# Kernel optimization log

Hardware: AMD Instinct MI355X
Metric: run time of the kernel (lower is better)

Reference implementation:

```python
import jax, jax.numpy as jnp
import numpy as np

B, N, D_IN, D, E, MAXD = 16, 512, 256, 64, 32, 50
LN_EPS = 1e-5

def setup_inputs() -> dict:
    key = jax.random.key(0)
    ks = jax.random.split(key, 24)
    s = lambda fan: 1.0 / np.sqrt(fan)
    inp = {
        'x': jax.random.normal(ks[0], (B, N, D_IN), jnp.float32),
        'price_rising_ranks': jax.random.randint(ks[1], (B, N), 0, N, jnp.int64),
        'Wp': jax.random.normal(ks[2], (D_IN, D), jnp.float32) * s(D_IN),
        'bp': jnp.zeros((D,), jnp.float32),
        'Wq': jax.random.normal(ks[3], (D, D), jnp.float32) * s(D),
        'bq': jnp.zeros((D,), jnp.float32),
        'Wk': jax.random.normal(ks[4], (D, D), jnp.float32) * s(D),
        'bk': jnp.zeros((D,), jnp.float32),
        'Wv': jax.random.normal(ks[5], (D, D), jnp.float32) * s(D),
        'bv': jnp.zeros((D,), jnp.float32),
        'Eemb': jax.random.normal(ks[6], (MAXD + 1, E), jnp.float32),
        'Wr1': jax.random.normal(ks[7], (E, 16), jnp.float32) * s(E),
        'br1': jnp.zeros((16,), jnp.float32),
        'Wr2': jax.random.normal(ks[8], (16, 1), jnp.float32) * s(16),
        'Wf1': jax.random.normal(ks[9], (D, 2 * D), jnp.float32) * s(D),
        'bf1': jnp.zeros((2 * D,), jnp.float32),
        'Wf2': jax.random.normal(ks[10], (2 * D, D), jnp.float32) * s(2 * D),
        'bf2': jnp.zeros((D,), jnp.float32),
        'ln_g': jnp.ones((D,), jnp.float32),
        'ln_b': jnp.zeros((D,), jnp.float32),
        'Ws1': jax.random.normal(ks[11], (D, 32), jnp.float32) * s(D),
        'bs1': jnp.zeros((32,), jnp.float32),
        'Ws2': jax.random.normal(ks[12], (32, 1), jnp.float32) * s(32),
        'bs2': jnp.zeros((1,), jnp.float32),
    }
    return inp

def reference(x, price_rising_ranks, Wp, bp, Wq, bq, Wk, bk, Wv, bv,
              Eemb, Wr1, br1, Wr2, Wf1, bf1, Wf2, bf2, ln_g, ln_b,
              Ws1, bs1, Ws2, bs2):
    xp = x @ Wp + bp                                  # (B,N,D)
    q = xp @ Wq + bq
    k = xp @ Wk + bk
    v = xp @ Wv + bv
    scores = jnp.einsum('bnd,bmd->bnm', q, k) / jnp.sqrt(jnp.float32(D))
    # rank-distance pairwise bias
    r = price_rising_ranks
    dists = jnp.clip(jnp.abs(r[:, :, None] - r[:, None, :]), 0, MAXD)  # (B,N,N) int
    emb = Eemb[dists]                                 # (B,N,N,E)
    w = jax.nn.relu(emb @ Wr1 + br1) @ Wr2            # (B,N,N,1)
    rel = jax.nn.sigmoid(w[..., 0])                   # (B,N,N)
    scores = scores * rel
    attn = jax.nn.softmax(scores, axis=-1)
    ao = jnp.einsum('bnm,bmd->bnd', attn, v)
    # feed forward + layernorm
    h = jax.nn.relu(ao @ Wf1 + bf1) @ Wf2 + bf2
    mu = jnp.mean(h, axis=-1, keepdims=True)
    var = jnp.mean((h - mu) ** 2, axis=-1, keepdims=True)
    hn = (h - mu) / jnp.sqrt(var + LN_EPS) * ln_g + ln_b
    # score projection
    out = jax.nn.relu(hn @ Ws1 + bs1) @ Ws2 + bs2     # (B,N,1)
    return jax.nn.sigmoid(out[..., 0])                # (B,N)
```

## Files before the change

### kernel.cpp

```cpp
#include <hip/hip_runtime.h>

using f32x4 = __attribute__((ext_vector_type(4))) float;
using s16x8 = __attribute__((ext_vector_type(8))) short;

static __device__ __forceinline__ unsigned short f2bf(float f){
  union { float f; unsigned int i; } c; c.f = f;
  return (unsigned short)((c.i + 0x7FFFu + ((c.i >> 16) & 1u)) >> 16);
}
static __device__ __forceinline__ s16x8 ld8(const unsigned short* p){
  return *(const s16x8*)p;
}
static __device__ __forceinline__ s16x8 cvt8(const float* p){
  const float4* q = (const float4*)p;
  float4 a = q[0], b = q[1];
  s16x8 r;
  r[0]=(short)f2bf(a.x); r[1]=(short)f2bf(a.y); r[2]=(short)f2bf(a.z); r[3]=(short)f2bf(a.w);
  r[4]=(short)f2bf(b.x); r[5]=(short)f2bf(b.y); r[6]=(short)f2bf(b.z); r[7]=(short)f2bf(b.w);
  return r;
}
static __device__ __forceinline__ f32x4 mfma16(s16x8 a, s16x8 b, f32x4 c){
  return __builtin_amdgcn_mfma_f32_16x16x32_bf16(a, b, c, 0, 0, 0);
}

__global__ __launch_bounds__(64) void k_prep(const float* __restrict__ Ee,
    const float* __restrict__ Wr1, const float* __restrict__ br1,
    const float* __restrict__ Wr2, float* __restrict__ rel_t)
{
  int t = threadIdx.x;
  if (t < 51){
    float e[32];
    for (int j = 0; j < 32; ++j) e[j] = Ee[t*32 + j];
    float w = 0.f;
    for (int h = 0; h < 16; ++h){
      float s = br1[h];
      for (int j = 0; j < 32; ++j) s += e[j] * Wr1[j*16 + h];
      s = fmaxf(s, 0.f);
      w += s * Wr2[h];
    }
    rel_t[t] = 1.f / (1.f + __expf(-w));
  }
}

__global__ __launch_bounds__(256) void k_xp(const float* __restrict__ x,
    const float* __restrict__ Wp, const float* __restrict__ bp,
    unsigned short* __restrict__ xp)
{
  __shared__ __align__(16) unsigned short Wt[64*264];
  int t = threadIdx.x;
  for (int i = t; i < 256*64; i += 256){
    int k = i >> 6, n = i & 63;
    Wt[n*264 + k] = f2bf(Wp[i]);
  }
  __syncthreads();
  int lane = t & 63, wave = t >> 6;
  int colL = lane & 15, quad = lane >> 4;
  int row0 = blockIdx.x * 64 + wave * 16;
  const float* xr = x + (row0 + colL)*256;
  f32x4 acc[4] = {};
  for (int kc = 0; kc < 256; kc += 32){
    s16x8 a = cvt8(xr + kc + quad*8);
#pragma unroll
    for (int nt = 0; nt < 4; ++nt){
      s16x8 b = ld8(&Wt[(nt*16 + colL)*264 + kc + quad*8]);
      acc[nt] = mfma16(a, b, acc[nt]);
    }
  }
#pragma unroll
  for (int nt = 0; nt < 4; ++nt){
    int col = nt*16 + colL;
    float bias = bp[col];
#pragma unroll
    for (int i = 0; i < 4; ++i){
      int row = row0 + quad*4 + i;
      xp[row*64 + col] = f2bf(acc[nt][i] + bias);
    }
  }
}

__global__ __launch_bounds__(256) void k_qkv(const unsigned short* __restrict__ xp,
    const float* __restrict__ Wq, const float* __restrict__ bq,
    const float* __restrict__ Wk, const float* __restrict__ bk,
    const float* __restrict__ Wv, const float* __restrict__ bv,
    unsigned short* __restrict__ q, unsigned short* __restrict__ k, unsigned short* __restrict__ vt)
{
  int which = blockIdx.y;
  const float* W    = which==0 ? Wq : (which==1 ? Wk : Wv);
  const float* bias = which==0 ? bq : (which==1 ? bk : bv);
  __shared__ __align__(16) unsigned short Wt[64*72];
  int t = threadIdx.x;
  for (int i = t; i < 64*64; i += 256){
    int kx = i >> 6, n = i & 63;
    Wt[n*72 + kx] = f2bf(W[i]);
  }
  __syncthreads();
  int lane = t & 63, wave = t >> 6;
  int colL = lane & 15, quad = lane >> 4;
  int row0 = blockIdx.x*64 + wave*16;
  f32x4 acc[4] = {};
#pragma unroll
  for (int kc = 0; kc < 64; kc += 32){
    s16x8 a = ld8(xp + (row0+colL)*64 + kc + quad*8);
#pragma unroll
    for (int nt = 0; nt < 4; ++nt){
      s16x8 b = ld8(&Wt[(nt*16+colL)*72 + kc + quad*8]);
      acc[nt] = mfma16(a, b, acc[nt]);
    }
  }
#pragma unroll
  for (int nt = 0; nt < 4; ++nt){
    int col = nt*16 + colL;
    float bb = bias[col];
#pragma unroll
    for (int i = 0; i < 4; ++i){
      int row = row0 + quad*4 + i;
      float v = acc[nt][i] + bb;
      if (which == 0)      q[row*64 + col] = f2bf(v);
      else if (which == 1) k[row*64 + col] = f2bf(v);
      else                 vt[(row>>9)*32768 + col*512 + (row & 511)] = f2bf(v);
    }
  }
}

__global__ __launch_bounds__(128) void k_attn(const unsigned short* __restrict__ q,
    const unsigned short* __restrict__ kmat, const unsigned short* __restrict__ vt,
    const int* __restrict__ ranks, const float* __restrict__ rel_t,
    unsigned short* __restrict__ ao)
{
  int b = blockIdx.y, qb = blockIdx.x;
  int t = threadIdx.x;
  int lane = t & 63, wave = t >> 6;
  int colL = lane & 15, quad = lane >> 4;

  __shared__ int r_s[512];
  __shared__ float rt_s[64];
  __shared__ __align__(16) unsigned short P[2][16*520];

  for (int i = t; i < 512; i += 128) r_s[i] = ranks[b*512 + i];
  if (t < 64) rt_s[t] = (t < 51) ? rel_t[t] : 0.f;
  __syncthreads();

  int row0 = qb*32 + wave*16;
  const unsigned short* qp = q    + b*512*64;
  const unsigned short* kp = kmat + b*512*64;
  const unsigned short* vp = vt   + b*64*512;

  s16x8 aq0 = ld8(qp + (row0+colL)*64 +  0 + quad*8);
  s16x8 aq1 = ld8(qp + (row0+colL)*64 + 32 + quad*8);

  f32x4 S[32];
#pragma unroll
  for (int mt = 0; mt < 32; ++mt){
    s16x8 b0 = ld8(kp + (mt*16+colL)*64 +  0 + quad*8);
    s16x8 b1 = ld8(kp + (mt*16+colL)*64 + 32 + quad*8);
    f32x4 c = {};
    c = mfma16(aq0, b0, c);
    c = mfma16(aq1, b1, c);
    S[mt] = c;
  }

  int rq[4];
#pragma unroll
  for (int i = 0; i < 4; ++i) rq[i] = r_s[row0 + quad*4 + i];

  float rmax[4] = {-1e30f,-1e30f,-1e30f,-1e30f};
#pragma unroll
  for (int mt = 0; mt < 32; ++mt){
    int rm = r_s[mt*16 + colL];
#pragma unroll
    for (int i = 0; i < 4; ++i){
      int dd = rq[i] - rm; dd = dd < 0 ? -dd : dd; dd = dd > 50 ? 50 : dd;
      float s = S[mt][i] * 0.125f * rt_s[dd];
      S[mt][i] = s;
      rmax[i] = fmaxf(rmax[i], s);
    }
  }
#pragma unroll
  for (int i = 0; i < 4; ++i){
    rmax[i] = fmaxf(rmax[i], __shfl_xor(rmax[i], 1));
    rmax[i] = fmaxf(rmax[i], __shfl_xor(rmax[i], 2));
    rmax[i] = fmaxf(rmax[i], __shfl_xor(rmax[i], 4));
    rmax[i] = fmaxf(rmax[i], __shfl_xor(rmax[i], 8));
  }
  float rsum[4] = {0.f,0.f,0.f,0.f};
#pragma unroll
  for (int mt = 0; mt < 32; ++mt){
#pragma unroll
    for (int i = 0; i < 4; ++i){
      float p = __expf(S[mt][i] - rmax[i]);
      S[mt][i] = p;
      rsum[i] += p;
    }
  }
#pragma unroll
  for (int i = 0; i < 4; ++i){
    rsum[i] += __shfl_xor(rsum[i], 1);
    rsum[i] += __shfl_xor(rsum[i], 2);
    rsum[i] += __shfl_xor(rsum[i], 4);
    rsum[i] += __shfl_xor(rsum[i], 8);
  }
  float inv[4];
#pragma unroll
  for (int i = 0; i < 4; ++i) inv[i] = 1.f / rsum[i];

  unsigned short* Pw = P[wave];
#pragma unroll
  for (int mt = 0; mt < 32; ++mt){
#pragma unroll
    for (int i = 0; i < 4; ++i)
      Pw[(quad*4+i)*520 + mt*16 + colL] = f2bf(S[mt][i] * inv[i]);
  }
  __syncthreads();

  f32x4 O[4] = {};
#pragma unroll
  for (int mc = 0; mc < 512; mc += 32){
    s16x8 ap = ld8(&Pw[colL*520 + mc + quad*8]);
#pragma unroll
    for (int dt = 0; dt < 4; ++dt){
      s16x8 bb = ld8(vp + (dt*16+colL)*512 + mc + quad*8);
      O[dt] = mfma16(ap, bb, O[dt]);
    }
  }
#pragma unroll
  for (int dt = 0; dt < 4; ++dt){
#pragma unroll
    for (int i = 0; i < 4; ++i)
      ao[(b*512 + row0 + quad*4 + i)*64 + dt*16 + colL] = f2bf(O[dt][i]);
  }
}

__global__ __launch_bounds__(256) void k_ffn(const unsigned short* __restrict__ ao,
    const float* __restrict__ Wf1, const float* __restrict__ bf1,
    const float* __restrict__ Wf2, const float* __restrict__ bf2,
    const float* __restrict__ lng, const float* __restrict__ lnb,
    const float* __restrict__ Ws1, const float* __restrict__ bs1,
    const float* __restrict__ Ws2, const float* __restrict__ bs2,
    float* __restrict__ out)
{
  __shared__ __align__(16) unsigned short Wf1t[128*72];
  __shared__ __align__(16) unsigned short Wf2t[64*136];
  __shared__ __align__(16) unsigned short Ws1t[32*72];
  __shared__ __align__(16) unsigned short hbuf[4][16*136];
  __shared__ float cb[384];

  int t = threadIdx.x;
  for (int i = t; i < 64*128; i += 256){ int d = i>>7, j = i&127; Wf1t[j*72 + d] = f2bf(Wf1[i]); }
  for (int i = t; i < 128*64; i += 256){ int kx = i>>6, n = i&63; Wf2t[n*136 + kx] = f2bf(Wf2[i]); }
  for (int i = t; i < 64*32;  i += 256){ int d = i>>5, c = i&31; Ws1t[c*72 + d] = f2bf(Ws1[i]); }
  if (t < 128) cb[t] = bf1[t];
  if (t < 64){ cb[128+t] = bf2[t]; cb[192+t] = lng[t]; cb[256+t] = lnb[t]; }
  if (t < 32){ cb[320+t] = bs1[t]; cb[352+t] = Ws2[t]; }
  __syncthreads();

  int lane = t & 63, wave = t >> 6, colL = lane & 15, quad = lane >> 4;
  int row0 = blockIdx.x*64 + wave*16;
  unsigned short* hw = hbuf[wave];

  f32x4 a1[8] = {};
#pragma unroll
  for (int kc = 0; kc < 64; kc += 32){
    s16x8 a = ld8(ao + (row0+colL)*64 + kc + quad*8);
#pragma unroll
    for (int nt = 0; nt < 8; ++nt){
      s16x8 b = ld8(&Wf1t[(nt*16+colL)*72 + kc + quad*8]);
      a1[nt] = mfma16(a, b, a1[nt]);
    }
  }
#pragma unroll
  for (int nt = 0; nt < 8; ++nt){
    int col = nt*16 + colL;
    float bb = cb[col];
#pragma unroll
    for (int i = 0; i < 4; ++i)
      hw[(quad*4+i)*136 + col] = f2bf(fmaxf(a1[nt][i] + bb, 0.f));
  }
  __syncthreads();

  f32x4 a2[4] = {};
#pragma unroll
  for (int kc = 0; kc < 128; kc += 32){
    s16x8 a = ld8(&hw[colL*136 + kc + quad*8]);
#pragma unroll
    for (int nt = 0; nt < 4; ++nt){
      s16x8 b = ld8(&Wf2t[(nt*16+colL)*136 + kc + quad*8]);
      a2[nt] = mfma16(a, b, a2[nt]);
    }
  }
  float vals[4][4];
#pragma unroll
  for (int nt = 0; nt < 4; ++nt){
    float bb = cb[128 + nt*16 + colL];
#pragma unroll
    for (int i = 0; i < 4; ++i) vals[i][nt] = a2[nt][i] + bb;
  }
  __syncthreads();

  float hnv[4][4];
#pragma unroll
  for (int i = 0; i < 4; ++i){
    float s = vals[i][0]+vals[i][1]+vals[i][2]+vals[i][3];
    s += __shfl_xor(s,1); s += __shfl_xor(s,2); s += __shfl_xor(s,4); s += __shfl_xor(s,8);
    float mu = s * (1.f/64.f);
    float d0=vals[i][0]-mu, d1=vals[i][1]-mu, d2=vals[i][2]-mu, d3=vals[i][3]-mu;
    float s2 = d0*d0 + d1*d1 + d2*d2 + d3*d3;
    s2 += __shfl_xor(s2,1); s2 += __shfl_xor(s2,2); s2 += __shfl_xor(s2,4); s2 += __shfl_xor(s2,8);
    float invs = rsqrtf(s2*(1.f/64.f) + 1e-5f);
#pragma unroll
    for (int nt = 0; nt < 4; ++nt){
      int col = nt*16 + colL;
      hnv[i][nt] = (vals[i][nt]-mu)*invs*cb[192+col] + cb[256+col];
    }
  }
#pragma unroll
  for (int i = 0; i < 4; ++i)
#pragma unroll
    for (int nt = 0; nt < 4; ++nt)
      hw[(quad*4+i)*72 + nt*16 + colL] = f2bf(hnv[i][nt]);
  __syncthreads();

  f32x4 a3[2] = {};
#pragma unroll
  for (int kc = 0; kc < 64; kc += 32){
    s16x8 a = ld8(&hw[colL*72 + kc + quad*8]);
#pragma unroll
    for (int nt = 0; nt < 2; ++nt){
      s16x8 b = ld8(&Ws1t[(nt*16+colL)*72 + kc + quad*8]);
      a3[nt] = mfma16(a, b, a3[nt]);
    }
  }
  float bs2f = bs2[0];
#pragma unroll
  for (int i = 0; i < 4; ++i){
    float p = 0.f;
#pragma unroll
    for (int nt = 0; nt < 2; ++nt){
      int col = nt*16 + colL;
      p += fmaxf(a3[nt][i] + cb[320+col], 0.f) * cb[352+col];
    }
    p += __shfl_xor(p,1); p += __shfl_xor(p,2); p += __shfl_xor(p,4); p += __shfl_xor(p,8);
    if (colL == 0){
      float z = p + bs2f;
      out[row0 + quad*4 + i] = 1.f / (1.f + __expf(-z));
    }
  }
}

extern "C" void kernel_launch(void* const* d_in, const int* in_sizes, int n_in,
                              void* d_out, int out_size, void* d_ws, size_t ws_size,
                              hipStream_t stream)
{
  const float* x    = (const float*)d_in[0];
  const int*   rank = (const int*)d_in[1];
  const float* Wp   = (const float*)d_in[2];
  const float* bp   = (const float*)d_in[3];
  const float* Wq   = (const float*)d_in[4];
  const float* bq   = (const float*)d_in[5];
  const float* Wk   = (const float*)d_in[6];
  const float* bk   = (const float*)d_in[7];
  const float* Wv   = (const float*)d_in[8];
  const float* bv   = (const float*)d_in[9];
  const float* Ee   = (const float*)d_in[10];
  const float* Wr1  = (const float*)d_in[11];
  const float* br1  = (const float*)d_in[12];
  const float* Wr2  = (const float*)d_in[13];
  const float* Wf1  = (const float*)d_in[14];
  const float* bf1  = (const float*)d_in[15];
  const float* Wf2  = (const float*)d_in[16];
  const float* bf2  = (const float*)d_in[17];
  const float* lng  = (const float*)d_in[18];
  const float* lnb  = (const float*)d_in[19];
  const float* Ws1  = (const float*)d_in[20];
  const float* bs1  = (const float*)d_in[21];
  const float* Ws2  = (const float*)d_in[22];
  const float* bs2  = (const float*)d_in[23];
  float* out = (float*)d_out;

  char* ws = (char*)d_ws;
  float*          rel_t = (float*)(ws + 0);
  unsigned short* xp    = (unsigned short*)(ws + 256);
  unsigned short* q     = (unsigned short*)(ws + 256 + 1*1048576);
  unsigned short* kk    = (unsigned short*)(ws + 256 + 2*1048576);
  unsigned short* vt    = (unsigned short*)(ws + 256 + 3*1048576);
  unsigned short* ao    = (unsigned short*)(ws + 256 + 4*1048576);

  k_prep<<<dim3(1), dim3(64), 0, stream>>>(Ee, Wr1, br1, Wr2, rel_t);
  k_xp<<<dim3(128), dim3(256), 0, stream>>>(x, Wp, bp, xp);
  k_qkv<<<dim3(128, 3), dim3(256), 0, stream>>>(xp, Wq, bq, Wk, bk, Wv, bv, q, kk, vt);
  k_attn<<<dim3(16, 16), dim3(128), 0, stream>>>(q, kk, vt, rank, rel_t, ao);
  k_ffn<<<dim3(128), dim3(256), 0, stream>>>(ao, Wf1, bf1, Wf2, bf2, lng, lnb,
                                             Ws1, bs1, Ws2, bs2, out);
}
```

Measured before the change: 151.8 us.

## Fuse projection, QKV and rel-table kernels; split attention keys across waves

```diff
diff --git a/kernel.cpp b/kernel.cpp
--- a/kernel.cpp
+++ b/kernel.cpp
@@ -22,150 +22,138 @@
   return __builtin_amdgcn_mfma_f32_16x16x32_bf16(a, b, c, 0, 0, 0);
 }
 
-__global__ __launch_bounds__(64) void k_prep(const float* __restrict__ Ee,
-    const float* __restrict__ Wr1, const float* __restrict__ br1,
-    const float* __restrict__ Wr2, float* __restrict__ rel_t)
+__global__ __launch_bounds__(128) void k_proj(const float* __restrict__ x,
+    const float* __restrict__ Wp, const float* __restrict__ bp,
+    const float* __restrict__ Wq, const float* __restrict__ bq,
+    const float* __restrict__ Wk, const float* __restrict__ bk,
+    const float* __restrict__ Wv, const float* __restrict__ bv,
+    const float* __restrict__ Ee, const float* __restrict__ Wr1,
+    const float* __restrict__ br1, const float* __restrict__ Wr2,
+    unsigned short* __restrict__ q, unsigned short* __restrict__ kk,
+    unsigned short* __restrict__ vt, float* __restrict__ rel_t)
 {
+  __shared__ __align__(16) unsigned short WpT[64*264];
+  __shared__ __align__(16) unsigned short Wt3[3][64*72];
+  __shared__ __align__(16) unsigned short xs[2][16*72];
+
   int t = threadIdx.x;
-  if (t < 51){
+  for (int i = t; i < 256*64; i += 128){
+    int k = i >> 6, n = i & 63;
+    WpT[n*264 + k] = f2bf(Wp[i]);
+  }
+  for (int i = t; i < 64*64; i += 128){
+    int k2 = i >> 6, n = i & 63;
+    Wt3[0][n*72 + k2] = f2bf(Wq[i]);
+    Wt3[1][n*72 + k2] = f2bf(Wk[i]);
+    Wt3[2][n*72 + k2] = f2bf(Wv[i]);
+  }
+  if (blockIdx.x == 0 && t < 51){
     float e[32];
     for (int j = 0; j < 32; ++j) e[j] = Ee[t*32 + j];
     float w = 0.f;
     for (int h = 0; h < 16; ++h){
       float s = br1[h];
       for (int j = 0; j < 32; ++j) s += e[j] * Wr1[j*16 + h];
-      s = fmaxf(s, 0.f);
-      w += s * Wr2[h];
+      w += fmaxf(s, 0.f) * Wr2[h];
     }
     rel_t[t] = 1.f / (1.f + __expf(-w));
   }
-}
-
-__global__ __launch_bounds__(256) void k_xp(const float* __restrict__ x,
-    const float* __restrict__ Wp, const float* __restrict__ bp,
-    unsigned short* __restrict__ xp)
-{
-  __shared__ __align__(16) unsigned short Wt[64*264];
-  int t = threadIdx.x;
-  for (int i = t; i < 256*64; i += 256){
-    int k = i >> 6, n = i & 63;
-    Wt[n*264 + k] = f2bf(Wp[i]);
-  }
-  __syncthreads();
-  int lane = t & 63, wave = t >> 6;
-  int colL = lane & 15, quad = lane >> 4;
-  int row0 = blockIdx.x * 64 + wave * 16;
+  __syncthreads();
+
+  int lane = t & 63, wave = t >> 6, colL = lane & 15, quad = lane >> 4;
+  int row0 = blockIdx.x*32 + wave*16;
+
   const float* xr = x + (row0 + colL)*256;
   f32x4 acc[4] = {};
   for (int kc = 0; kc < 256; kc += 32){
     s16x8 a = cvt8(xr + kc + quad*8);
 #pragma unroll
-    for (int nt = 0; nt < 4; ++nt){
-      s16x8 b = ld8(&Wt[(nt*16 + colL)*264 + kc + quad*8]);
-      acc[nt] = mfma16(a, b, acc[nt]);
-    }
-  }
+    for (int nt = 0; nt < 4; ++nt)
+      acc[nt] = mfma16(a, ld8(&WpT[(nt*16+colL)*264 + kc + quad*8]), acc[nt]);
+  }
+  unsigned short* xw = xs[wave];
 #pragma unroll
   for (int nt = 0; nt < 4; ++nt){
     int col = nt*16 + colL;
-    float bias = bp[col];
-#pragma unroll
-    for (int i = 0; i < 4; ++i){
-      int row = row0 + quad*4 + i;
-      xp[row*64 + col] = f2bf(acc[nt][i] + bias);
-    }
-  }
-}
-
-__global__ __launch_bounds__(256) void k_qkv(const unsigned short* __restrict__ xp,
-    const float* __restrict__ Wq, const float* __restrict__ bq,
-    const float* __restrict__ Wk, const float* __restrict__ bk,
-    const float* __restrict__ Wv, const float* __restrict__ bv,
-    unsigned short* __restrict__ q, unsigned short* __restrict__ k, unsigned short* __restrict__ vt)
-{
-  int which = blockIdx.y;
-  const float* W    = which==0 ? Wq : (which==1 ? Wk : Wv);
-  const float* bias = which==0 ? bq : (which==1 ? bk : bv);
-  __shared__ __align__(16) unsigned short Wt[64*72];
-  int t = threadIdx.x;
-  for (int i = t; i < 64*64; i += 256){
-    int kx = i >> 6, n = i & 63;
-    Wt[n*72 + kx] = f2bf(W[i]);
-  }
-  __syncthreads();
-  int lane = t & 63, wave = t >> 6;
-  int colL = lane & 15, quad = lane >> 4;
-  int row0 = blockIdx.x*64 + wave*16;
-  f32x4 acc[4] = {};
-#pragma unroll
-  for (int kc = 0; kc < 64; kc += 32){
-    s16x8 a = ld8(xp + (row0+colL)*64 + kc + quad*8);
+    float bb = bp[col];
+#pragma unroll
+    for (int i = 0; i < 4; ++i)
+      xw[(quad*4+i)*72 + col] = f2bf(acc[nt][i] + bb);
+  }
+  s16x8 a0 = ld8(&xw[colL*72 +  0 + quad*8]);
+  s16x8 a1 = ld8(&xw[colL*72 + 32 + quad*8]);
+
+#pragma unroll
+  for (int w = 0; w < 3; ++w){
+    const float* bias = w==0 ? bq : (w==1 ? bk : bv);
+    f32x4 c[4] = {};
 #pragma unroll
     for (int nt = 0; nt < 4; ++nt){
-      s16x8 b = ld8(&Wt[(nt*16+colL)*72 + kc + quad*8]);
-      acc[nt] = mfma16(a, b, acc[nt]);
-    }
-  }
-#pragma unroll
-  for (int nt = 0; nt < 4; ++nt){
-    int col = nt*16 + colL;
-    float bb = bias[col];
-#pragma unroll
-    for (int i = 0; i < 4; ++i){
-      int row = row0 + quad*4 + i;
-      float v = acc[nt][i] + bb;
-      if (which == 0)      q[row*64 + col] = f2bf(v);
-      else if (which == 1) k[row*64 + col] = f2bf(v);
-      else                 vt[(row>>9)*32768 + col*512 + (row & 511)] = f2bf(v);
-    }
-  }
-}
-
-__global__ __launch_bounds__(128) void k_attn(const unsigned short* __restrict__ q,
+      c[nt] = mfma16(a0, ld8(&Wt3[w][(nt*16+colL)*72 +  0 + quad*8]), c[nt]);
+      c[nt] = mfma16(a1, ld8(&Wt3[w][(nt*16+colL)*72 + 32 + quad*8]), c[nt]);
+    }
+#pragma unroll
+    for (int nt = 0; nt < 4; ++nt){
+      int col = nt*16 + colL;
+      float bb = bias[col];
+#pragma unroll
+      for (int i = 0; i < 4; ++i){
+        int row = row0 + quad*4 + i;
+        float v = c[nt][i] + bb;
+        if (w == 0)      q [row*64 + col] = f2bf(v);
+        else if (w == 1) kk[row*64 + col] = f2bf(v);
+        else             vt[(row>>9)*32768 + col*512 + (row & 511)] = f2bf(v);
+      }
+    }
+  }
+}
+
+__global__ __launch_bounds__(256) void k_attn(const unsigned short* __restrict__ q,
     const unsigned short* __restrict__ kmat, const unsigned short* __restrict__ vt,
     const int* __restrict__ ranks, const float* __restrict__ rel_t,
     unsigned short* __restrict__ ao)
 {
-  int b = blockIdx.y, qb = blockIdx.x;
-  int t = threadIdx.x;
-  int lane = t & 63, wave = t >> 6;
+  int b = blockIdx.y, qt = blockIdx.x;
+  int t = threadIdx.x, lane = t & 63, wave = t >> 6;
   int colL = lane & 15, quad = lane >> 4;
 
   __shared__ int r_s[512];
   __shared__ float rt_s[64];
-  __shared__ __align__(16) unsigned short P[2][16*520];
-
-  for (int i = t; i < 512; i += 128) r_s[i] = ranks[b*512 + i];
+  __shared__ __align__(16) unsigned short P[4][16*136];
+  __shared__ float Opart[4][16*66];
+  __shared__ float pmax_s[4][16], psum_s[4][16];
+
+  for (int i = t; i < 512; i += 256) r_s[i] = ranks[b*512 + i];
   if (t < 64) rt_s[t] = (t < 51) ? rel_t[t] : 0.f;
   __syncthreads();
 
-  int row0 = qb*32 + wave*16;
-  const unsigned short* qp = q    + b*512*64;
-  const unsigned short* kp = kmat + b*512*64;
-  const unsigned short* vp = vt   + b*64*512;
-
-  s16x8 aq0 = ld8(qp + (row0+colL)*64 +  0 + quad*8);
-  s16x8 aq1 = ld8(qp + (row0+colL)*64 + 32 + quad*8);
-
-  f32x4 S[32];
-#pragma unroll
-  for (int mt = 0; mt < 32; ++mt){
-    s16x8 b0 = ld8(kp + (mt*16+colL)*64 +  0 + quad*8);
-    s16x8 b1 = ld8(kp + (mt*16+colL)*64 + 32 + quad*8);
+  int qrow0 = qt*16;
+  const unsigned short* qp = q    + b*32768;
+  const unsigned short* kp = kmat + b*32768;
+  const unsigned short* vp = vt   + b*32768;
+
+  s16x8 aq0 = ld8(qp + (qrow0+colL)*64 +  0 + quad*8);
+  s16x8 aq1 = ld8(qp + (qrow0+colL)*64 + 32 + quad*8);
+
+  int key0 = wave*128;
+  f32x4 S[8];
+#pragma unroll
+  for (int mt = 0; mt < 8; ++mt){
+    int key = key0 + mt*16 + colL;
     f32x4 c = {};
-    c = mfma16(aq0, b0, c);
-    c = mfma16(aq1, b1, c);
+    c = mfma16(aq0, ld8(kp + key*64 +  0 + quad*8), c);
+    c = mfma16(aq1, ld8(kp + key*64 + 32 + quad*8), c);
     S[mt] = c;
   }
 
   int rq[4];
 #pragma unroll
-  for (int i = 0; i < 4; ++i) rq[i] = r_s[row0 + quad*4 + i];
+  for (int i = 0; i < 4; ++i) rq[i] = r_s[qrow0 + quad*4 + i];
 
   float rmax[4] = {-1e30f,-1e30f,-1e30f,-1e30f};
 #pragma unroll
-  for (int mt = 0; mt < 32; ++mt){
-    int rm = r_s[mt*16 + colL];
+  for (int mt = 0; mt < 8; ++mt){
+    int rm = r_s[key0 + mt*16 + colL];
 #pragma unroll
     for (int i = 0; i < 4; ++i){
       int dd = rq[i] - rm; dd = dd < 0 ? -dd : dd; dd = dd > 50 ? 50 : dd;
@@ -181,12 +169,23 @@
     rmax[i] = fmaxf(rmax[i], __shfl_xor(rmax[i], 4));
     rmax[i] = fmaxf(rmax[i], __shfl_xor(rmax[i], 8));
   }
+  if (colL == 0){
+#pragma unroll
+    for (int i = 0; i < 4; ++i) pmax_s[wave][quad*4 + i] = rmax[i];
+  }
+  __syncthreads();
+  float gmax[4];
+#pragma unroll
+  for (int i = 0; i < 4; ++i){
+    int r = quad*4 + i;
+    gmax[i] = fmaxf(fmaxf(pmax_s[0][r], pmax_s[1][r]), fmaxf(pmax_s[2][r], pmax_s[3][r]));
+  }
   float rsum[4] = {0.f,0.f,0.f,0.f};
 #pragma unroll
-  for (int mt = 0; mt < 32; ++mt){
+  for (int mt = 0; mt < 8; ++mt){
 #pragma unroll
     for (int i = 0; i < 4; ++i){
-      float p = __expf(S[mt][i] - rmax[i]);
+      float p = __expf(S[mt][i] - gmax[i]);
       S[mt][i] = p;
       rsum[i] += p;
     }
@@ -198,38 +197,48 @@
     rsum[i] += __shfl_xor(rsum[i], 4);
     rsum[i] += __shfl_xor(rsum[i], 8);
   }
+  if (colL == 0){
+#pragma unroll
+    for (int i = 0; i < 4; ++i) psum_s[wave][quad*4 + i] = rsum[i];
+  }
+  __syncthreads();
   float inv[4];
 #pragma unroll
-  for (int i = 0; i < 4; ++i) inv[i] = 1.f / rsum[i];
-
+  for (int i = 0; i < 4; ++i){
+    int r = quad*4 + i;
+    inv[i] = 1.f / (psum_s[0][r] + psum_s[1][r] + psum_s[2][r] + psum_s[3][r]);
+  }
   unsigned short* Pw = P[wave];
 #pragma unroll
-  for (int mt = 0; mt < 32; ++mt){
+  for (int mt = 0; mt < 8; ++mt){
 #pragma unroll
     for (int i = 0; i < 4; ++i)
-      Pw[(quad*4+i)*520 + mt*16 + colL] = f2bf(S[mt][i] * inv[i]);
-  }
-  __syncthreads();
-
+      Pw[(quad*4+i)*136 + mt*16 + colL] = f2bf(S[mt][i] * inv[i]);
+  }
   f32x4 O[4] = {};
 #pragma unroll
-  for (int mc = 0; mc < 512; mc += 32){
-    s16x8 ap = ld8(&Pw[colL*520 + mc + quad*8]);
-#pragma unroll
-    for (int dt = 0; dt < 4; ++dt){
-      s16x8 bb = ld8(vp + (dt*16+colL)*512 + mc + quad*8);
-      O[dt] = mfma16(ap, bb, O[dt]);
-    }
-  }
-#pragma unroll
-  for (int dt = 0; dt < 4; ++dt){
+  for (int mc = 0; mc < 128; mc += 32){
+    s16x8 ap = ld8(&Pw[colL*136 + mc + quad*8]);
+#pragma unroll
+    for (int dt = 0; dt < 4; ++dt)
+      O[dt] = mfma16(ap, ld8(vp + (dt*16+colL)*512 + key0 + mc + quad*8), O[dt]);
+  }
+  float* Ow = Opart[wave];
+#pragma unroll
+  for (int dt = 0; dt < 4; ++dt)
 #pragma unroll
     for (int i = 0; i < 4; ++i)
-      ao[(b*512 + row0 + quad*4 + i)*64 + dt*16 + colL] = f2bf(O[dt][i]);
-  }
-}
-
-__global__ __launch_bounds__(256) void k_ffn(const unsigned short* __restrict__ ao,
+      Ow[(quad*4+i)*66 + dt*16 + colL] = O[dt][i];
+  __syncthreads();
+  for (int e = t; e < 1024; e += 256){
+    int row = e >> 6, col = e & 63;
+    float s = Opart[0][row*66+col] + Opart[1][row*66+col]
+            + Opart[2][row*66+col] + Opart[3][row*66+col];
+    ao[(b*512 + qrow0 + row)*64 + col] = f2bf(s);
+  }
+}
+
+__global__ __launch_bounds__(128) void k_ffn(const unsigned short* __restrict__ ao,
     const float* __restrict__ Wf1, const float* __restrict__ bf1,
     const float* __restrict__ Wf2, const float* __restrict__ bf2,
     const float* __restrict__ lng, const float* __restrict__ lnb,
@@ -240,20 +249,20 @@
   __shared__ __align__(16) unsigned short Wf1t[128*72];
   __shared__ __align__(16) unsigned short Wf2t[64*136];
   __shared__ __align__(16) unsigned short Ws1t[32*72];
-  __shared__ __align__(16) unsigned short hbuf[4][16*136];
+  __shared__ __align__(16) unsigned short hbuf[2][16*136];
   __shared__ float cb[384];
 
   int t = threadIdx.x;
-  for (int i = t; i < 64*128; i += 256){ int d = i>>7, j = i&127; Wf1t[j*72 + d] = f2bf(Wf1[i]); }
-  for (int i = t; i < 128*64; i += 256){ int kx = i>>6, n = i&63; Wf2t[n*136 + kx] = f2bf(Wf2[i]); }
-  for (int i = t; i < 64*32;  i += 256){ int d = i>>5, c = i&31; Ws1t[c*72 + d] = f2bf(Ws1[i]); }
+  for (int i = t; i < 64*128; i += 128){ int d = i>>7, j = i&127; Wf1t[j*72 + d] = f2bf(Wf1[i]); }
+  for (int i = t; i < 128*64; i += 128){ int kx = i>>6, n = i&63; Wf2t[n*136 + kx] = f2bf(Wf2[i]); }
+  for (int i = t; i < 64*32;  i += 128){ int d = i>>5, c = i&31; Ws1t[c*72 + d] = f2bf(Ws1[i]); }
   if (t < 128) cb[t] = bf1[t];
   if (t < 64){ cb[128+t] = bf2[t]; cb[192+t] = lng[t]; cb[256+t] = lnb[t]; }
   if (t < 32){ cb[320+t] = bs1[t]; cb[352+t] = Ws2[t]; }
   __syncthreads();
 
   int lane = t & 63, wave = t >> 6, colL = lane & 15, quad = lane >> 4;
-  int row0 = blockIdx.x*64 + wave*16;
+  int row0 = blockIdx.x*32 + wave*16;
   unsigned short* hw = hbuf[wave];
 
   f32x4 a1[8] = {};
@@ -261,10 +270,8 @@
   for (int kc = 0; kc < 64; kc += 32){
     s16x8 a = ld8(ao + (row0+colL)*64 + kc + quad*8);
 #pragma unroll
-    for (int nt = 0; nt < 8; ++nt){
-      s16x8 b = ld8(&Wf1t[(nt*16+colL)*72 + kc + quad*8]);
-      a1[nt] = mfma16(a, b, a1[nt]);
-    }
+    for (int nt = 0; nt < 8; ++nt)
+      a1[nt] = mfma16(a, ld8(&Wf1t[(nt*16+colL)*72 + kc + quad*8]), a1[nt]);
   }
 #pragma unroll
   for (int nt = 0; nt < 8; ++nt){
@@ -274,17 +281,13 @@
     for (int i = 0; i < 4; ++i)
       hw[(quad*4+i)*136 + col] = f2bf(fmaxf(a1[nt][i] + bb, 0.f));
   }
-  __syncthreads();
-
   f32x4 a2[4] = {};
 #pragma unroll
   for (int kc = 0; kc < 128; kc += 32){
     s16x8 a = ld8(&hw[colL*136 + kc + quad*8]);
 #pragma unroll
-    for (int nt = 0; nt < 4; ++nt){
-      s16x8 b = ld8(&Wf2t[(nt*16+colL)*136 + kc + quad*8]);
-      a2[nt] = mfma16(a, b, a2[nt]);
-    }
+    for (int nt = 0; nt < 4; ++nt)
+      a2[nt] = mfma16(a, ld8(&Wf2t[(nt*16+colL)*136 + kc + quad*8]), a2[nt]);
   }
   float vals[4][4];
 #pragma unroll
@@ -293,8 +296,6 @@
 #pragma unroll
     for (int i = 0; i < 4; ++i) vals[i][nt] = a2[nt][i] + bb;
   }
-  __syncthreads();
-
   float hnv[4][4];
 #pragma unroll
   for (int i = 0; i < 4; ++i){
@@ -316,17 +317,14 @@
 #pragma unroll
     for (int nt = 0; nt < 4; ++nt)
       hw[(quad*4+i)*72 + nt*16 + colL] = f2bf(hnv[i][nt]);
-  __syncthreads();
 
   f32x4 a3[2] = {};
 #pragma unroll
   for (int kc = 0; kc < 64; kc += 32){
     s16x8 a = ld8(&hw[colL*72 + kc + quad*8]);
 #pragma unroll
-    for (int nt = 0; nt < 2; ++nt){
-      s16x8 b = ld8(&Ws1t[(nt*16+colL)*72 + kc + quad*8]);
-      a3[nt] = mfma16(a, b, a3[nt]);
-    }
+    for (int nt = 0; nt < 2; ++nt)
+      a3[nt] = mfma16(a, ld8(&Ws1t[(nt*16+colL)*72 + kc + quad*8]), a3[nt]);
   }
   float bs2f = bs2[0];
 #pragma unroll
@@ -377,16 +375,14 @@
 
   char* ws = (char*)d_ws;
   float*          rel_t = (float*)(ws + 0);
-  unsigned short* xp    = (unsigned short*)(ws + 256);
-  unsigned short* q     = (unsigned short*)(ws + 256 + 1*1048576);
-  unsigned short* kk    = (unsigned short*)(ws + 256 + 2*1048576);
-  unsigned short* vt    = (unsigned short*)(ws + 256 + 3*1048576);
-  unsigned short* ao    = (unsigned short*)(ws + 256 + 4*1048576);
-
-  k_prep<<<dim3(1), dim3(64), 0, stream>>>(Ee, Wr1, br1, Wr2, rel_t);
-  k_xp<<<dim3(128), dim3(256), 0, stream>>>(x, Wp, bp, xp);
-  k_qkv<<<dim3(128, 3), dim3(256), 0, stream>>>(xp, Wq, bq, Wk, bk, Wv, bv, q, kk, vt);
-  k_attn<<<dim3(16, 16), dim3(128), 0, stream>>>(q, kk, vt, rank, rel_t, ao);
-  k_ffn<<<dim3(128), dim3(256), 0, stream>>>(ao, Wf1, bf1, Wf2, bf2, lng, lnb,
+  unsigned short* q     = (unsigned short*)(ws + 256);
+  unsigned short* kk    = (unsigned short*)(ws + 256 + 1*1048576);
+  unsigned short* vt    = (unsigned short*)(ws + 256 + 2*1048576);
+  unsigned short* ao    = (unsigned short*)(ws + 256 + 3*1048576);
+
+  k_proj<<<dim3(256), dim3(128), 0, stream>>>(x, Wp, bp, Wq, bq, Wk, bk, Wv, bv,
+                                              Ee, Wr1, br1, Wr2, q, kk, vt, rel_t);
+  k_attn<<<dim3(32, 16), dim3(256), 0, stream>>>(q, kk, vt, rank, rel_t, ao);
+  k_ffn<<<dim3(256), dim3(128), 0, stream>>>(ao, Wf1, bf1, Wf2, bf2, lng, lnb,
                                              Ws1, bs1, Ws2, bs2, out);
 }
```

After: 147.3 us. -2.9%, faster.
